# Optimization experiments

Measured on AMD Instinct MI355X. Metric: run time of the kernel, lower is better.

Reference implementation:

```python
import jax, jax.numpy as jnp
import numpy as np
from jax import lax

# The external iir2d op (fyremael/iir2d, filter_id=4) is a channel-wise recursive 2D IIR
# filter. We model it faithfully as the canonical separable zero-phase first-order IIR
# (causal then anticausal recurrence along W, then along H), with 'mirror' boundary
# handled by steady-state init (y[-1] = x[0]) and 'const' boundary by border_const.
A_DECAY = 0.5  # first-order feedback coefficient for filter_id=4


def _causal(x_t, c0, a):
    # x_t: (L, ...), scan a first-order recurrence y[t] = (1-a)*x[t] + a*y[t-1]
    b = 1.0 - a

    def step(carry, xt):
        y = b * xt + a * carry
        return y, y

    _, y = lax.scan(step, c0, x_t)
    return y


def _iir1d_last(x, a, border, border_const):
    # zero-phase: causal pass then anticausal pass along the last axis
    x_t = jnp.moveaxis(x, -1, 0)  # (L, ...)
    if border == 'mirror':
        c0 = x_t[0]
    else:
        c0 = jnp.full_like(x_t[0], border_const)
    yf = _causal(x_t, c0, a)
    yr = yf[::-1]
    if border == 'mirror':
        c1 = yr[0]
    else:
        c1 = jnp.full_like(yr[0], border_const)
    yb = _causal(yr, c1, a)[::-1]
    return jnp.moveaxis(yb, 0, -1)


def iir2d(x2d, a, border, border_const):
    # x2d: (M, H, W). Filter along W, then along H.
    y = _iir1d_last(x2d, a, border, border_const)  # rows (W axis)
    y = jnp.swapaxes(y, 1, 2)                       # (M, W, H)
    y = _iir1d_last(y, a, border, border_const)     # columns (H axis)
    return jnp.swapaxes(y, 1, 2)


def setup_inputs() -> dict:
    key = jax.random.key(0)
    kx = jax.random.fold_in(key, 1)
    x = jax.random.normal(kx, (4, 512, 512, 64), dtype=jnp.float32)
    alpha = jnp.zeros((64,), dtype=jnp.float32)  # learnable blend, init 0 => mix = 0.5
    return {"x": x, "alpha": alpha}


def reference(x, alpha):
    # y = x + sigmoid(alpha) * (IIR(x) - x), channel-wise IIR on NHWC
    n, h, w, c = x.shape
    x2d = jnp.transpose(x, (0, 3, 1, 2)).reshape((n * c, h, w))
    y2d = iir2d(x2d, A_DECAY, 'mirror', 0.0)
    y = jnp.transpose(y2d.reshape((n, c, h, w)), (0, 2, 3, 1))
    mix = jax.nn.sigmoid(alpha).reshape((1, 1, 1, -1))
    return x + mix * (y - x)
```

## Files before the change

kernel.cpp:

```cpp
#include <hip/hip_runtime.h>


typedef float f2 __attribute__((ext_vector_type(2)));

constexpr int Tc   = 32;
constexpr int Kc   = 8;
constexpr int WIN  = Tc + 2 * Kc;
constexpr int L    = 512;
constexpr int C    = 64;
constexpr int W    = 512;
constexpr int H    = 512;
constexpr int CHUNKS = L / Tc;

template<bool VERT, bool COMBINE>
__global__ __launch_bounds__(256)
void iir_scan(const float* __restrict__ in, float* __restrict__ out,
              const float* __restrict__ xres, const float* __restrict__ alpha)
{
    const int nb8 = (int)gridDim.x >> 3;
    const int bid = (int)blockIdx.x;
    const int lb  = (bid & 7) * nb8 + (bid >> 3);

    const int lane = threadIdx.x & 63;
    const int sub  = lane >> 5;
    const int c0   = (lane & 31) << 1;
    const int gw   = lb * 4 + (threadIdx.x >> 6);
    const int lg   = gw >> 4;
    const int w0   = (gw & (CHUNKS - 1)) * Tc;

    const int n = lg >> 8;
    const int r = ((lg & 255) << 1) + sub;

    int base, stride;
    if (VERT) {
        base   = (n * H * W + r) * C + c0;
        stride = W * C;
    } else {
        base   = (n * H + r) * (W * C) + c0;
        stride = C;
    }
    const float* __restrict__ p = in + base;

    f2 v[WIN];
#pragma unroll
    for (int j = 0; j < WIN; ++j) {
        int w = w0 - Kc + j;
        w = min(max(w, 0), L - 1);
        v[j] = *(const f2*)(p + w * stride);
    }

    f2 carry = v[0];
#pragma unroll
    for (int j = 0; j < WIN; ++j) {
        const int w = w0 - Kc + j;
        if (w >= 0 && w < L)
            carry = 0.5f * v[j] + 0.5f * carry;
        v[j] = carry;
    }

    f2 c2 = v[WIN - 1];
#pragma unroll
    for (int j = WIN - 1; j >= Kc; --j) {
        c2 = 0.5f * v[j] + 0.5f * c2;
        v[j] = c2;
    }

    if (COMBINE) {
        const f2 av = *(const f2*)(alpha + c0);
        f2 mix;
#pragma unroll
        for (int q = 0; q < 2; ++q)
            mix[q] = 1.0f / (1.0f + __expf(-av[q]));
#pragma unroll
        for (int j = Kc; j < Kc + Tc; ++j) {
            const int idx = base + (w0 + (j - Kc)) * stride;
            const f2 xv = *(const f2*)(xres + idx);
            *(f2*)(out + idx) = xv + mix * (v[j] - xv);
        }
    } else {
#pragma unroll
        for (int j = Kc; j < Kc + Tc; ++j) {
            const int idx = base + (w0 + (j - Kc)) * stride;
            *(f2*)(out + idx) = v[j];
        }
    }
}

__global__ __launch_bounds__(256)
void iir_vpass_inplace(float* __restrict__ y, const float* __restrict__ xres,
                       const float* __restrict__ alpha)
{
    const int lane = threadIdx.x & 63;
    const int sub  = lane >> 5;
    const int c0   = (lane & 31) << 1;
    const int lg   = blockIdx.x * 4 + (threadIdx.x >> 6);
    const int n = lg >> 8;
    const int w = ((lg & 255) << 1) + sub;
    const int base   = (n * H * W + w) * C + c0;
    const int stride = W * C;

    f2 carry = *(const f2*)(y + base);
    for (int h = 0; h < H; ++h) {
        const int idx = base + h * stride;
        f2 cur = *(const f2*)(y + idx);
        carry = 0.5f * cur + 0.5f * carry;
        *(f2*)(y + idx) = carry;
    }
    const f2 av = *(const f2*)(alpha + c0);
    f2 mix;
#pragma unroll
    for (int q = 0; q < 2; ++q)
        mix[q] = 1.0f / (1.0f + __expf(-av[q]));
    f2 c2 = *(const f2*)(y + base + (H - 1) * stride);
    for (int h = H - 1; h >= 0; --h) {
        const int idx = base + h * stride;
        f2 cur = *(const f2*)(y + idx);
        c2 = 0.5f * cur + 0.5f * c2;
        const f2 xv = *(const f2*)(xres + idx);
        *(f2*)(y + idx) = xv + mix * (c2 - xv);
    }
}

extern "C" void kernel_launch(void* const* d_in, const int* in_sizes, int n_in,
                              void* d_out, int out_size, void* d_ws, size_t ws_size,
                              hipStream_t stream) {
    const float* x     = (const float*)d_in[0];
    const float* alpha = (const float*)d_in[1];
    float* out = (float*)d_out;
    float* t   = (float*)d_ws;

    const size_t imgElems = (size_t)H * W * C;
    const size_t imgBytes = imgElems * sizeof(float);
    const int    N        = 4;

    int g = (int)(ws_size / imgBytes);
    if (g > N) g = N;

    if (g >= 1) {
        for (int i0 = 0; i0 < N; i0 += g) {
            const int ni = (i0 + g <= N) ? g : (N - i0);
            const size_t off = (size_t)i0 * imgElems;
            const dim3 grid((unsigned)(ni * 1024)), block(256);
            iir_scan<false, false><<<grid, block, 0, stream>>>(x + off, t, nullptr, nullptr);
            iir_scan<true,  true ><<<grid, block, 0, stream>>>(t, out + off, x + off, alpha);
        }
    } else {
        const dim3 block(256);
        iir_scan<false, false><<<dim3(4 * 1024), block, 0, stream>>>(x, out, nullptr, nullptr);
        iir_vpass_inplace<<<dim3(256), block, 0, stream>>>(out, x, alpha);
    }
}
```

Baseline: 605.9 us.

## Stage IIR chunk windows into LDS via direct global-to-LDS DMA loads

Replaces the templated register-window scan kernel with separate horizontal and vertical kernels. Each one loads its overlapping chunk window into shared memory through global_load_lds 16-byte DMA and then runs the causal and anticausal recurrences out of LDS, one channel per lane. The thread mapping changes from two channels per lane to one channel per lane with the grid doubled. The aim is to cut vector register pressure, coalesce loads into wide 16-byte accesses, and trim halo work at the image borders, at the cost of LDS round trips and scalar 4-byte stores.

Measured after the change: 711.6 us. 17.4% more time.

```diff
diff --git a/kernel.cpp b/kernel.cpp
--- a/kernel.cpp
+++ b/kernel.cpp
@@ -1,7 +1,5 @@
 #include <hip/hip_runtime.h>
 
-
-typedef float f2 __attribute__((ext_vector_type(2)));
 
 constexpr int Tc   = 32;
 constexpr int Kc   = 8;
@@ -12,76 +10,113 @@
 constexpr int H    = 512;
 constexpr int CHUNKS = L / Tc;
 
-template<bool VERT, bool COMBINE>
+typedef float f2 __attribute__((ext_vector_type(2)));
+
+__device__ __forceinline__ void dma16(const float* g, float* l) {
+    __builtin_amdgcn_global_load_lds(
+        (const __attribute__((address_space(1))) unsigned int*)g,
+        (__attribute__((address_space(3))) unsigned int*)l,
+        16, 0, 0);
+}
+
 __global__ __launch_bounds__(256)
-void iir_scan(const float* __restrict__ in, float* __restrict__ out,
-              const float* __restrict__ xres, const float* __restrict__ alpha)
+void iir_h(const float* __restrict__ in, float* __restrict__ out)
 {
+    __shared__ float lds[4][WIN * 64];
+
     const int nb8 = (int)gridDim.x >> 3;
     const int bid = (int)blockIdx.x;
     const int lb  = (bid & 7) * nb8 + (bid >> 3);
 
+    const int wv   = threadIdx.x >> 6;
     const int lane = threadIdx.x & 63;
-    const int sub  = lane >> 5;
-    const int c0   = (lane & 31) << 1;
-    const int gw   = lb * 4 + (threadIdx.x >> 6);
-    const int lg   = gw >> 4;
-    const int w0   = (gw & (CHUNKS - 1)) * Tc;
+    const int chunk = lb & (CHUNKS - 1);
+    const int hq    = (lb >> 4) & 127;
+    const int n     = lb >> 11;
+    const int h     = hq * 4 + wv;
+    const int w0    = chunk * Tc;
 
-    const int n = lg >> 8;
-    const int r = ((lg & 255) << 1) + sub;
+    const int v0  = max(0, w0 - Kc);
+    const int v1  = min(L, w0 + Tc + Kc);
+    const int cnt = v1 - v0;
+    const int nkb = cnt >> 2;
 
-    int base, stride;
-    if (VERT) {
-        base   = (n * H * W + r) * C + c0;
-        stride = W * C;
-    } else {
-        base   = (n * H + r) * (W * C) + c0;
-        stride = C;
-    }
-    const float* __restrict__ p = in + base;
+    const float* lbase = in + ((size_t)(n * H + h)) * W * C + v0 * C;
+    float* Wl = &lds[wv][0];
 
-    f2 v[WIN];
-#pragma unroll
-    for (int j = 0; j < WIN; ++j) {
-        int w = w0 - Kc + j;
-        w = min(max(w, 0), L - 1);
-        v[j] = *(const f2*)(p + w * stride);
+    for (int i = 0; i < nkb; ++i)
+        dma16(lbase + i * 256 + lane * 4, Wl + i * 256);
+    asm volatile("s_waitcnt vmcnt(0)" ::: "memory");
+    __builtin_amdgcn_sched_barrier(0);
+
+    float carry = Wl[lane];
+    for (int s = 0; s < cnt; ++s) {
+        const float x = Wl[s * 64 + lane];
+        carry = 0.5f * x + 0.5f * carry;
+        Wl[s * 64 + lane] = carry;
     }
 
-    f2 carry = v[0];
-#pragma unroll
-    for (int j = 0; j < WIN; ++j) {
-        const int w = w0 - Kc + j;
-        if (w >= 0 && w < L)
-            carry = 0.5f * v[j] + 0.5f * carry;
-        v[j] = carry;
+    float c2 = carry;
+    const int sOutLo = w0 - v0;
+    float* obase = out + ((size_t)(n * H + h)) * W * C;
+    for (int s = cnt - 1; s >= sOutLo; --s) {
+        const float yf = Wl[s * 64 + lane];
+        c2 = 0.5f * yf + 0.5f * c2;
+        const int p = v0 + s;
+        if (p < w0 + Tc)
+            obase[p * C + lane] = c2;
+    }
+}
+
+__global__ __launch_bounds__(256)
+void iir_v(const float* __restrict__ in, float* __restrict__ out,
+           const float* __restrict__ xres, const float* __restrict__ alpha)
+{
+    __shared__ float lds[WIN * 256];
+
+    const int nb8 = (int)gridDim.x >> 3;
+    const int bid = (int)blockIdx.x;
+    const int lb  = (bid & 7) * nb8 + (bid >> 3);
+
+    const int wv   = threadIdx.x >> 6;
+    const int lane = threadIdx.x & 63;
+    const int chunk = lb & (CHUNKS - 1);
+    const int wg    = (lb >> 4) & 127;
+    const int n     = lb >> 11;
+    const int w0    = chunk * Tc;
+
+    const int v0  = max(0, w0 - Kc);
+    const int v1  = min(L, w0 + Tc + Kc);
+    const int cnt = v1 - v0;
+
+    const float* nbase = in + (size_t)n * H * W * C;
+
+    for (int i = wv; i < cnt; i += 4)
+        dma16(nbase + (size_t)(v0 + i) * W * C + wg * 256 + lane * 4,
+              &lds[i * 256]);
+    asm volatile("s_waitcnt vmcnt(0)" ::: "memory");
+    __syncthreads();
+
+    float* Wl = &lds[wv * 64];
+    float carry = Wl[lane];
+    for (int s = 0; s < cnt; ++s) {
+        const float x = Wl[s * 256 + lane];
+        carry = 0.5f * x + 0.5f * carry;
+        Wl[s * 256 + lane] = carry;
     }
 
-    f2 c2 = v[WIN - 1];
-#pragma unroll
-    for (int j = WIN - 1; j >= Kc; --j) {
-        c2 = 0.5f * v[j] + 0.5f * c2;
-        v[j] = c2;
-    }
-
-    if (COMBINE) {
-        const f2 av = *(const f2*)(alpha + c0);
-        f2 mix;
-#pragma unroll
-        for (int q = 0; q < 2; ++q)
-            mix[q] = 1.0f / (1.0f + __expf(-av[q]));
-#pragma unroll
-        for (int j = Kc; j < Kc + Tc; ++j) {
-            const int idx = base + (w0 + (j - Kc)) * stride;
-            const f2 xv = *(const f2*)(xres + idx);
-            *(f2*)(out + idx) = xv + mix * (v[j] - xv);
-        }
-    } else {
-#pragma unroll
-        for (int j = Kc; j < Kc + Tc; ++j) {
-            const int idx = base + (w0 + (j - Kc)) * stride;
-            *(f2*)(out + idx) = v[j];
+    const float mix = 1.0f / (1.0f + __expf(-alpha[lane]));
+    float c2 = carry;
+    const int sOutLo = w0 - v0;
+    const size_t colbase = (size_t)n * H * W * C + (size_t)(wg * 4 + wv) * C + lane;
+    for (int s = cnt - 1; s >= sOutLo; --s) {
+        const float yf = Wl[s * 256 + lane];
+        c2 = 0.5f * yf + 0.5f * c2;
+        const int p = v0 + s;
+        if (p < w0 + Tc) {
+            const size_t idx = colbase + (size_t)p * W * C;
+            const float xv = xres[idx];
+            out[idx] = xv + mix * (c2 - xv);
         }
     }
 }
@@ -140,13 +175,13 @@
         for (int i0 = 0; i0 < N; i0 += g) {
             const int ni = (i0 + g <= N) ? g : (N - i0);
             const size_t off = (size_t)i0 * imgElems;
-            const dim3 grid((unsigned)(ni * 1024)), block(256);
-            iir_scan<false, false><<<grid, block, 0, stream>>>(x + off, t, nullptr, nullptr);
-            iir_scan<true,  true ><<<grid, block, 0, stream>>>(t, out + off, x + off, alpha);
+            const dim3 grid((unsigned)(ni * 2048)), block(256);
+            iir_h<<<grid, block, 0, stream>>>(x + off, t);
+            iir_v<<<grid, block, 0, stream>>>(t, out + off, x + off, alpha);
         }
     } else {
         const dim3 block(256);
-        iir_scan<false, false><<<dim3(4 * 1024), block, 0, stream>>>(x, out, nullptr, nullptr);
+        iir_h<<<dim3(4 * 2048), block, 0, stream>>>(x, out);
         iir_vpass_inplace<<<dim3(256), block, 0, stream>>>(out, x, alpha);
     }
 }
```
